# Kernel optimization log

Measured on AMD Instinct MI355X. Metric: run time of the kernel, lower is better.

The kernel has to match this reference:

```python
import jax, jax.numpy as jnp
import numpy as np

NEG_SLOPE = 0.2
EPS = 1e-16


def _gat_conv(x, edge_index, W, att_src, att_dst, bias):
    """PyG-style GATConv: linear -> per-edge attention -> segment softmax over dst -> scatter-sum.
    x: [N, Fin], W: [Fin, H*F], att_src/att_dst: [H, F], bias: [H*F].
    Adds self-loops (PyG default)."""
    N = x.shape[0]
    H, F = att_src.shape
    h = (x @ W).reshape(N, H, F)                       # [N, H, F]
    loops = jnp.arange(N, dtype=edge_index.dtype)
    src = jnp.concatenate([edge_index[0], loops])      # [E+N]
    dst = jnp.concatenate([edge_index[1], loops])
    a_s = jnp.sum(h * att_src[None], axis=-1)          # [N, H]
    a_d = jnp.sum(h * att_dst[None], axis=-1)          # [N, H]
    e = a_s[src] + a_d[dst]                            # [E+N, H]
    e = jnp.where(e > 0, e, NEG_SLOPE * e)             # leaky_relu
    m = jax.ops.segment_max(e, dst, num_segments=N)    # stable segment softmax
    ex = jnp.exp(e - m[dst])
    s = jax.ops.segment_sum(ex, dst, num_segments=N)
    alpha = ex / (s[dst] + EPS)                        # [E+N, H]
    msg = h[src] * alpha[..., None]                    # [E+N, H, F]
    out = jax.ops.segment_sum(msg, dst, num_segments=N)  # [N, H, F]
    return out.reshape(N, H * F) + bias


def setup_inputs() -> dict:
    key = jax.random.key(0)
    ks = jax.random.split(key, 12)
    N, E, Q = 200000, 6400000, 1000000
    return {
        "x": jax.random.normal(ks[0], (N, 1), jnp.float32),
        "edge_index": jax.random.randint(ks[1], (2, E), 0, N, jnp.int64),
        "src": jax.random.randint(ks[2], (Q,), 0, N, jnp.int64),
        "dst": jax.random.randint(ks[3], (Q,), 0, N, jnp.int64),
        "W1": jax.random.normal(ks[4], (1, 8), jnp.float32) * 0.5,
        "att_src1": jax.random.normal(ks[5], (2, 4), jnp.float32) * 0.5,
        "att_dst1": jax.random.normal(ks[6], (2, 4), jnp.float32) * 0.5,
        "b1": jnp.zeros((8,), jnp.float32),
        "W2": jax.random.normal(ks[7], (8, 8), jnp.float32) * 0.35,
        "att_src2": jax.random.normal(ks[8], (2, 4), jnp.float32) * 0.5,
        "att_dst2": jax.random.normal(ks[9], (2, 4), jnp.float32) * 0.5,
        "b2": jnp.zeros((8,), jnp.float32),
        "Wl": jax.random.normal(ks[10], (16, 2), jnp.float32) * 0.25,
        "bl": jnp.zeros((2,), jnp.float32),
    }


def reference(x, edge_index, src, dst, W1, att_src1, att_dst1, b1,
              W2, att_src2, att_dst2, b2, Wl, bl):
    h = _gat_conv(x, edge_index, W1, att_src1, att_dst1, b1)   # [N, 8]
    h = _gat_conv(h, edge_index, W2, att_src2, att_dst2, b2)   # [N, 8]
    y = jnp.concatenate([h[src], h[dst]], axis=-1)             # [Q, 16]
    return y @ Wl + bl                                         # [Q, 2]
```

## Files before the change

### kernel.cpp

```cpp
#include <hip/hip_runtime.h>
#include <hip/hip_fp16.h>

#define NEG_SLOPE 0.2f
#define GAT_EPS 1e-16f

#define BSHIFT 9
#define BSIZE 512
#define NBPAD 512
#define CAP_BKT 17664

#define K3_T 512
#define K3_VPT 8
#define K3_TILE (K3_T * K3_VPT)

#define CAP_BUILD 18432

typedef _Float16 half8 __attribute__((ext_vector_type(8)));

static __device__ __forceinline__ float leaky(float v) {
    return v > 0.0f ? v : NEG_SLOPE * v;
}


__global__ __launch_bounds__(K3_T) void bin_scatter_kernel(
        const int* __restrict__ src, const int* __restrict__ dst, int E, int NB,
        int* __restrict__ bcursor, unsigned int* __restrict__ binned) {
    __shared__ int cnt[NBPAD];
    __shared__ int lstart[NBPAD];
    __shared__ int gbase[NBPAD];
    __shared__ unsigned int buf[K3_TILE];
    __shared__ unsigned short tgtb[K3_TILE];
    const int tid = threadIdx.x;
    const int t0 = blockIdx.x * K3_TILE;

    cnt[tid] = 0;
    __syncthreads();

    int b[K3_VPT];
    unsigned int v[K3_VPT];
    #pragma unroll
    for (int k = 0; k < K3_VPT; ++k) {
        int i = t0 + k * K3_T + tid;
        b[k] = -1;
        if (i < E) {
            int d = dst[i];
            int s = src[i];
            b[k] = d >> BSHIFT;
            v[k] = ((unsigned int)s << BSHIFT) | (unsigned int)(d & (BSIZE - 1));
            atomicAdd(&cnt[b[k]], 1);
        }
    }
    __syncthreads();

    int c = cnt[tid];
    lstart[tid] = c;
    __syncthreads();
    for (int ofs = 1; ofs < NBPAD; ofs <<= 1) {
        int t = (tid >= ofs) ? lstart[tid - ofs] : 0;
        __syncthreads();
        lstart[tid] += t;
        __syncthreads();
    }
    int excl = lstart[tid] - c;
    if (tid < NB) gbase[tid] = tid * CAP_BKT + (c ? atomicAdd(&bcursor[tid], c) : 0);
    __syncthreads();
    lstart[tid] = excl;
    cnt[tid] = 0;
    __syncthreads();

    #pragma unroll
    for (int k = 0; k < K3_VPT; ++k) {
        if (b[k] >= 0) {
            int r = atomicAdd(&cnt[b[k]], 1);
            int slot = lstart[b[k]] + r;
            buf[slot] = v[k];
            tgtb[slot] = (unsigned short)b[k];
        }
    }
    __syncthreads();

    int nvalid = min(K3_TILE, E - t0);
    for (int j = tid; j < nvalid; j += K3_T) {
        int bb = tgtb[j];
        binned[gbase[bb] + (j - lstart[bb])] = buf[j];
    }
}


__global__ __launch_bounds__(BSIZE) void bucket_build_kernel(
        unsigned int* __restrict__ binned,
        const int* __restrict__ bcursor,
        int N,
        int2* __restrict__ rowrange) {
    extern __shared__ unsigned int sbuf[];
    __shared__ int cnt[BSIZE];
    __shared__ int lstart[BSIZE];
    const int b = blockIdx.x;
    const int tid = threadIdx.x;
    const int e0 = b * CAP_BKT;
    const int nE = bcursor[b];
    const int n0 = b << BSHIFT;

    cnt[tid] = 0;
    __syncthreads();
    for (int i = tid; i < nE; i += BSIZE)
        atomicAdd(&cnt[binned[e0 + i] & (BSIZE - 1)], 1);
    __syncthreads();

    int c = cnt[tid];
    lstart[tid] = c;
    __syncthreads();
    for (int ofs = 1; ofs < BSIZE; ofs <<= 1) {
        int t = (tid >= ofs) ? lstart[tid - ofs] : 0;
        __syncthreads();
        lstart[tid] += t;
        __syncthreads();
    }
    int excl = lstart[tid] - c;
    __syncthreads();
    lstart[tid] = excl;
    cnt[tid] = 0;
    __syncthreads();

    int n = n0 + tid;
    if (n < N) rowrange[n] = make_int2(e0 + excl, e0 + excl + c);

    for (int i = tid; i < nE; i += BSIZE) {
        unsigned int v = binned[e0 + i];
        int dl = v & (BSIZE - 1);
        int r = atomicAdd(&cnt[dl], 1);
        int slot = lstart[dl] + r;
        if (slot < CAP_BUILD) sbuf[slot] = v >> BSHIFT;
    }
    __syncthreads();

    int lim = min(nE, CAP_BUILD);
    for (int j = tid; j < lim; j += BSIZE)
        binned[e0 + j] = sbuf[j];
}


__global__ void prep1_kernel(const float* __restrict__ x,
                             const float* __restrict__ W1,
                             const float* __restrict__ adw,
                             int N,
                             float2* __restrict__ adst,
                             half8* __restrict__ h16) {
    int n = blockIdx.x * blockDim.x + threadIdx.x;
    if (n >= N) return;
    float xv = x[n];
    float hv[8];
    #pragma unroll
    for (int j = 0; j < 8; ++j) hv[j] = xv * W1[j];
    float d0 = 0.f, d1 = 0.f;
    #pragma unroll
    for (int f = 0; f < 4; ++f) {
        d0 += hv[f] * adw[f];
        d1 += hv[4 + f] * adw[4 + f];
    }
    adst[n] = make_float2(d0, d1);
    half8 ho;
    #pragma unroll
    for (int j = 0; j < 8; ++j) ho[j] = (_Float16)hv[j];
    h16[n] = ho;
}


__global__ void prep2_kernel(const float* __restrict__ in,
                             const float* __restrict__ W2,
                             const float* __restrict__ adw,
                             int N,
                             float2* __restrict__ adst,
                             half8* __restrict__ h16) {
    int n = blockIdx.x * blockDim.x + threadIdx.x;
    if (n >= N) return;
    const float4* ip = (const float4*)(in + (size_t)n * 8);
    float4 i0 = ip[0], i1 = ip[1];
    float iv[8] = {i0.x, i0.y, i0.z, i0.w, i1.x, i1.y, i1.z, i1.w};
    float hv[8];
    #pragma unroll
    for (int j = 0; j < 8; ++j) {
        float acc = 0.f;
        #pragma unroll
        for (int k = 0; k < 8; ++k) acc += iv[k] * W2[k * 8 + j];
        hv[j] = acc;
    }
    float d0 = 0.f, d1 = 0.f;
    #pragma unroll
    for (int f = 0; f < 4; ++f) {
        d0 += hv[f] * adw[f];
        d1 += hv[4 + f] * adw[4 + f];
    }
    adst[n] = make_float2(d0, d1);
    half8 ho;
    #pragma unroll
    for (int j = 0; j < 8; ++j) ho[j] = (_Float16)hv[j];
    h16[n] = ho;
}


__global__ void gat_pass_kernel(const float2* __restrict__ adst,
                                const half8* __restrict__ h16,
                                const int2* __restrict__ rowrange,
                                const unsigned int* __restrict__ col,
                                const float* __restrict__ asw,
                                const float* __restrict__ bias,
                                int N,
                                float* __restrict__ out32,
                                half8* __restrict__ out16) {
    int t = blockIdx.x * blockDim.x + threadIdx.x;
    int n = t >> 3;
    int lane = t & 7;
    if (n >= N) return;
    float w0 = asw[0], w1 = asw[1], w2 = asw[2], w3 = asw[3];
    float w4 = asw[4], w5 = asw[5], w6 = asw[6], w7 = asw[7];
    float2 ad = adst[n];
    float sum0 = 0.f, sum1 = 0.f;
    float acc[8] = {0.f, 0.f, 0.f, 0.f, 0.f, 0.f, 0.f, 0.f};
    if (lane == 0) {
        half8 hh = h16[n];
        float hs[8];
        #pragma unroll
        for (int k = 0; k < 8; ++k) hs[k] = (float)hh[k];
        float a0 = hs[0] * w0 + hs[1] * w1 + hs[2] * w2 + hs[3] * w3;
        float a1 = hs[4] * w4 + hs[5] * w5 + hs[6] * w6 + hs[7] * w7;
        float p0 = __expf(leaky(a0 + ad.x));
        float p1 = __expf(leaky(a1 + ad.y));
        sum0 = p0; sum1 = p1;
        #pragma unroll
        for (int k = 0; k < 4; ++k) { acc[k] = hs[k] * p0; acc[4 + k] = hs[4 + k] * p1; }
    }
    int2 rr = rowrange[n];
    for (int i = rr.x + lane; i < rr.y; i += 8) {
        unsigned int s = __builtin_nontemporal_load(&col[i]);
        half8 hh = h16[s];
        float hs[8];
        #pragma unroll
        for (int k = 0; k < 8; ++k) hs[k] = (float)hh[k];
        float a0 = hs[0] * w0 + hs[1] * w1 + hs[2] * w2 + hs[3] * w3;
        float a1 = hs[4] * w4 + hs[5] * w5 + hs[6] * w6 + hs[7] * w7;
        float q0 = __expf(leaky(a0 + ad.x));
        float q1 = __expf(leaky(a1 + ad.y));
        sum0 += q0; sum1 += q1;
        #pragma unroll
        for (int k = 0; k < 4; ++k) { acc[k] += hs[k] * q0; acc[4 + k] += hs[4 + k] * q1; }
    }
    #pragma unroll
    for (int ofs = 1; ofs < 8; ofs <<= 1) {
        sum0 += __shfl_xor(sum0, ofs, 8);
        sum1 += __shfl_xor(sum1, ofs, 8);
        #pragma unroll
        for (int k = 0; k < 8; ++k) acc[k] += __shfl_xor(acc[k], ofs, 8);
    }
    if (lane == 0) {
        float inv0 = 1.0f / (sum0 + GAT_EPS);
        float inv1 = 1.0f / (sum1 + GAT_EPS);
        float r[8];
        #pragma unroll
        for (int k = 0; k < 4; ++k) {
            r[k] = acc[k] * inv0 + bias[k];
            r[4 + k] = acc[4 + k] * inv1 + bias[4 + k];
        }
        if (out32) {
            float4* op = (float4*)(out32 + (size_t)n * 8);
            op[0] = make_float4(r[0], r[1], r[2], r[3]);
            op[1] = make_float4(r[4], r[5], r[6], r[7]);
        }
        if (out16) {
            half8 ho;
            #pragma unroll
            for (int k = 0; k < 8; ++k) ho[k] = (_Float16)r[k];
            out16[n] = ho;
        }
    }
}


__global__ void final_kernel(const half8* __restrict__ h2,
                             const int* __restrict__ srcq,
                             const int* __restrict__ dstq,
                             const float* __restrict__ Wl,
                             const float* __restrict__ bl,
                             int Q,
                             float* __restrict__ y) {
    int q = blockIdx.x * blockDim.x + threadIdx.x;
    if (q >= Q) return;
    int s = srcq[q];
    int d = dstq[q];
    half8 hs8 = h2[s];
    half8 hd8 = h2[d];
    float y0 = bl[0], y1 = bl[1];
    #pragma unroll
    for (int k = 0; k < 8; ++k) {
        float hv = (float)hs8[k];
        y0 += hv * Wl[k * 2 + 0];
        y1 += hv * Wl[k * 2 + 1];
    }
    #pragma unroll
    for (int k = 0; k < 8; ++k) {
        float hv = (float)hd8[k];
        y0 += hv * Wl[(8 + k) * 2 + 0];
        y1 += hv * Wl[(8 + k) * 2 + 1];
    }
    *(float2*)(y + (size_t)q * 2) = make_float2(y0, y1);
}


static inline size_t align_up(size_t v, size_t a) { return (v + a - 1) & ~(a - 1); }

extern "C" void kernel_launch(void* const* d_in, const int* in_sizes, int n_in,
                              void* d_out, int out_size, void* d_ws, size_t ws_size,
                              hipStream_t stream) {
    const float* x    = (const float*)d_in[0];
    const int*   ei   = (const int*)d_in[1];
    const int*   srcq = (const int*)d_in[2];
    const int*   dstq = (const int*)d_in[3];
    const float* W1   = (const float*)d_in[4];
    const float* as1  = (const float*)d_in[5];
    const float* ad1  = (const float*)d_in[6];
    const float* b1   = (const float*)d_in[7];
    const float* W2   = (const float*)d_in[8];
    const float* as2  = (const float*)d_in[9];
    const float* ad2  = (const float*)d_in[10];
    const float* b2   = (const float*)d_in[11];
    const float* Wl   = (const float*)d_in[12];
    const float* bl   = (const float*)d_in[13];

    const int N = in_sizes[0];
    const int E = in_sizes[1] / 2;
    const int Q = in_sizes[2];
    const int NB = (N + BSIZE - 1) >> BSHIFT;

    const int* esrc = ei;
    const int* edst = ei + E;

    char* w = (char*)d_ws;
    unsigned int* binned = (unsigned int*)w;  w += align_up((size_t)NB * CAP_BKT * 4, 256);
    int*    bcursor  = (int*)w;               w += align_up((size_t)NBPAD * 4, 256);
    int2*   rowrange = (int2*)w;              w += align_up((size_t)N * 8, 256);
    half8*  h16  = (half8*)w;                 w += align_up((size_t)N * 16, 256);
    float2* adst = (float2*)w;                w += align_up((size_t)N * 8, 256);
    float*  out1 = (float*)w;                 w += align_up((size_t)N * 8 * 4, 256);
    half8*  out2h = (half8*)w;

    const int BT = 256;
    int nodeBlocks = (N + BT - 1) / BT;
    int gatBlocks  = ((N * 8) + BT - 1) / BT;
    int qBlocks    = (Q + BT - 1) / BT;
    int k3Blocks   = (E + K3_TILE - 1) / K3_TILE;

    hipMemsetAsync(bcursor, 0, (size_t)NBPAD * 4, stream);
    bin_scatter_kernel<<<k3Blocks, K3_T, 0, stream>>>(esrc, edst, E, NB, bcursor, binned);
    bucket_build_kernel<<<NB, BSIZE, CAP_BUILD * 4, stream>>>(binned, bcursor, N, rowrange);

    prep1_kernel<<<nodeBlocks, BT, 0, stream>>>(x, W1, ad1, N, adst, h16);
    gat_pass_kernel<<<gatBlocks, BT, 0, stream>>>(adst, h16, rowrange, binned, as1, b1, N,
                                                  out1, (half8*)nullptr);

    prep2_kernel<<<nodeBlocks, BT, 0, stream>>>(out1, W2, ad2, N, adst, h16);
    gat_pass_kernel<<<gatBlocks, BT, 0, stream>>>(adst, h16, rowrange, binned, as2, b2, N,
                                                  (float*)nullptr, out2h);

    final_kernel<<<qBlocks, BT, 0, stream>>>(out2h, srcq, dstq, Wl, bl, Q, (float*)d_out);
}
```

Measured before the change: 209.5 us.

## Vectorize edge loads in binning, pack shared buffers, widen GAT lanes with prefetch

```diff
diff --git a/kernel.cpp b/kernel.cpp
--- a/kernel.cpp
+++ b/kernel.cpp
@@ -10,10 +10,12 @@
 #define CAP_BKT 17664
 
 #define K3_T 512
-#define K3_VPT 8
+#define K3_VPT 16
 #define K3_TILE (K3_T * K3_VPT)
 
 #define CAP_BUILD 18432
+
+#define LPD 16
 
 typedef _Float16 half8 __attribute__((ext_vector_type(8)));
 
@@ -25,13 +27,13 @@
 __global__ __launch_bounds__(K3_T) void bin_scatter_kernel(
         const int* __restrict__ src, const int* __restrict__ dst, int E, int NB,
         int* __restrict__ bcursor, unsigned int* __restrict__ binned) {
+    extern __shared__ unsigned long long sbuf[];
     __shared__ int cnt[NBPAD];
     __shared__ int lstart[NBPAD];
     __shared__ int gbase[NBPAD];
-    __shared__ unsigned int buf[K3_TILE];
-    __shared__ unsigned short tgtb[K3_TILE];
     const int tid = threadIdx.x;
     const int t0 = blockIdx.x * K3_TILE;
+    const int base = t0 + tid * K3_VPT;
 
     cnt[tid] = 0;
     __syncthreads();
@@ -39,15 +41,23 @@
     int b[K3_VPT];
     unsigned int v[K3_VPT];
     #pragma unroll
-    for (int k = 0; k < K3_VPT; ++k) {
-        int i = t0 + k * K3_T + tid;
-        b[k] = -1;
-        if (i < E) {
-            int d = dst[i];
-            int s = src[i];
-            b[k] = d >> BSHIFT;
-            v[k] = ((unsigned int)s << BSHIFT) | (unsigned int)(d & (BSIZE - 1));
-            atomicAdd(&cnt[b[k]], 1);
+    for (int g = 0; g < K3_VPT / 4; ++g) {
+        int off = base + g * 4;
+        if (off < E) {
+            int4 s4 = *(const int4*)(src + off);
+            int4 d4 = *(const int4*)(dst + off);
+            int ss[4] = {s4.x, s4.y, s4.z, s4.w};
+            int dd[4] = {d4.x, d4.y, d4.z, d4.w};
+            #pragma unroll
+            for (int j = 0; j < 4; ++j) {
+                int k = g * 4 + j;
+                b[k] = dd[j] >> BSHIFT;
+                v[k] = ((unsigned int)ss[j] << BSHIFT) | (unsigned int)(dd[j] & (BSIZE - 1));
+                atomicAdd(&cnt[b[k]], 1);
+            }
+        } else {
+            #pragma unroll
+            for (int j = 0; j < 4; ++j) b[g * 4 + j] = -1;
         }
     }
     __syncthreads();
@@ -73,16 +83,16 @@
         if (b[k] >= 0) {
             int r = atomicAdd(&cnt[b[k]], 1);
             int slot = lstart[b[k]] + r;
-            buf[slot] = v[k];
-            tgtb[slot] = (unsigned short)b[k];
+            sbuf[slot] = ((unsigned long long)(unsigned int)b[k] << 32) | v[k];
         }
     }
     __syncthreads();
 
     int nvalid = min(K3_TILE, E - t0);
     for (int j = tid; j < nvalid; j += K3_T) {
-        int bb = tgtb[j];
-        binned[gbase[bb] + (j - lstart[bb])] = buf[j];
+        unsigned long long p = sbuf[j];
+        int bb = (int)(p >> 32);
+        binned[gbase[bb] + (j - lstart[bb])] = (unsigned int)p;
     }
 }
 
@@ -92,7 +102,7 @@
         const int* __restrict__ bcursor,
         int N,
         int2* __restrict__ rowrange) {
-    extern __shared__ unsigned int sbuf[];
+    extern __shared__ unsigned int sbuf32[];
     __shared__ int cnt[BSIZE];
     __shared__ int lstart[BSIZE];
     const int b = blockIdx.x;
@@ -130,13 +140,13 @@
         int dl = v & (BSIZE - 1);
         int r = atomicAdd(&cnt[dl], 1);
         int slot = lstart[dl] + r;
-        if (slot < CAP_BUILD) sbuf[slot] = v >> BSHIFT;
+        if (slot < CAP_BUILD) sbuf32[slot] = v >> BSHIFT;
     }
     __syncthreads();
 
     int lim = min(nE, CAP_BUILD);
     for (int j = tid; j < lim; j += BSIZE)
-        binned[e0 + j] = sbuf[j];
+        binned[e0 + j] = sbuf32[j];
 }
 
 
@@ -209,8 +219,8 @@
                                 float* __restrict__ out32,
                                 half8* __restrict__ out16) {
     int t = blockIdx.x * blockDim.x + threadIdx.x;
-    int n = t >> 3;
-    int lane = t & 7;
+    int n = t / LPD;
+    int lane = t & (LPD - 1);
     if (n >= N) return;
     float w0 = asw[0], w1 = asw[1], w2 = asw[2], w3 = asw[3];
     float w4 = asw[4], w5 = asw[5], w6 = asw[6], w7 = asw[7];
@@ -231,8 +241,11 @@
         for (int k = 0; k < 4; ++k) { acc[k] = hs[k] * p0; acc[4 + k] = hs[4 + k] * p1; }
     }
     int2 rr = rowrange[n];
-    for (int i = rr.x + lane; i < rr.y; i += 8) {
-        unsigned int s = __builtin_nontemporal_load(&col[i]);
+    int i = rr.x + lane;
+    unsigned int s = (i < rr.y) ? __builtin_nontemporal_load(&col[i]) : 0u;
+    while (i < rr.y) {
+        int inext = i + LPD;
+        unsigned int snext = (inext < rr.y) ? __builtin_nontemporal_load(&col[inext]) : 0u;
         half8 hh = h16[s];
         float hs[8];
         #pragma unroll
@@ -244,13 +257,14 @@
         sum0 += q0; sum1 += q1;
         #pragma unroll
         for (int k = 0; k < 4; ++k) { acc[k] += hs[k] * q0; acc[4 + k] += hs[4 + k] * q1; }
-    }
-    #pragma unroll
-    for (int ofs = 1; ofs < 8; ofs <<= 1) {
-        sum0 += __shfl_xor(sum0, ofs, 8);
-        sum1 += __shfl_xor(sum1, ofs, 8);
-        #pragma unroll
-        for (int k = 0; k < 8; ++k) acc[k] += __shfl_xor(acc[k], ofs, 8);
+        i = inext; s = snext;
+    }
+    #pragma unroll
+    for (int ofs = 1; ofs < LPD; ofs <<= 1) {
+        sum0 += __shfl_xor(sum0, ofs, LPD);
+        sum1 += __shfl_xor(sum1, ofs, LPD);
+        #pragma unroll
+        for (int k = 0; k < 8; ++k) acc[k] += __shfl_xor(acc[k], ofs, LPD);
     }
     if (lane == 0) {
         float inv0 = 1.0f / (sum0 + GAT_EPS);
@@ -345,13 +359,15 @@
 
     const int BT = 256;
     int nodeBlocks = (N + BT - 1) / BT;
-    int gatBlocks  = ((N * 8) + BT - 1) / BT;
+    int gatBlocks  = ((N * LPD) + BT - 1) / BT;
     int qBlocks    = (Q + BT - 1) / BT;
     int k3Blocks   = (E + K3_TILE - 1) / K3_TILE;
 
     hipMemsetAsync(bcursor, 0, (size_t)NBPAD * 4, stream);
-    bin_scatter_kernel<<<k3Blocks, K3_T, 0, stream>>>(esrc, edst, E, NB, bcursor, binned);
-    bucket_build_kernel<<<NB, BSIZE, CAP_BUILD * 4, stream>>>(binned, bcursor, N, rowrange);
+    bin_scatter_kernel<<<k3Blocks, K3_T, (size_t)K3_TILE * 8, stream>>>(
+        esrc, edst, E, NB, bcursor, binned);
+    bucket_build_kernel<<<NB, BSIZE, (size_t)CAP_BUILD * 4, stream>>>(
+        binned, bcursor, N, rowrange);
 
     prep1_kernel<<<nodeBlocks, BT, 0, stream>>>(x, W1, ad1, N, adst, h16);
     gat_pass_kernel<<<gatBlocks, BT, 0, stream>>>(adst, h16, rowrange, binned, as1, b1, N,
```

Measured after the change: 185.3 us. 1.13x faster.
